# Optimization experiments

Hardware: AMD Instinct MI355X
Metric: run time of the kernel (lower is better)

## Reference

```python
import jax, jax.numpy as jnp
import numpy as np

HID = 16  # hidden channels of each lifting subnet (P and U)


def _conv(x, W, b):
    # x: [N,1|HID,h,w], W: [O,I,3,3] -> SAME conv, NCHW
    y = jax.lax.conv_general_dilated(x, W, (1, 1), 'SAME',
                                     dimension_numbers=('NCHW', 'OIHW', 'NCHW'))
    return y + b[None, :, None, None]


def _subnet(x, W1, b1, W2, b2):
    return _conv(jax.nn.relu(_conv(x, W1, b1)), W2, b2)


def _lift(L, H, p, u):
    # predict/update lifting step: H -= P(L); L += U(H)
    H = H - _subnet(L, *p)
    L = L + _subnet(H, *u)
    return L, H


def _rgb2yuv(x):
    # [B,3,H,W] -> YUV, then channels folded into batch -> [3B,1,H,W]
    M = jnp.array([[0.299, 0.587, 0.114],
                   [-0.147, -0.289, 0.436],
                   [0.615, -0.515, -0.100]], dtype=x.dtype)
    y = jnp.einsum('cd,bdhw->bchw', M, x)
    B, C, H, W = y.shape
    return y.transpose(1, 0, 2, 3).reshape(C * B, 1, H, W)


def _batch2channel(x, C):
    # [C*B,1,h,w] -> [B,C,h,w]  (inverse of the batch-fold above)
    CB, _, h, w = x.shape
    B = CB // C
    return x.reshape(C, B, h, w).transpose(1, 0, 2, 3)


def setup_inputs():
    key = jax.random.key(0)
    ks = jax.random.split(key, 5)
    B, H, W = 8, 512, 512
    x = jax.random.normal(ks[0], (B, 3, H, W), jnp.float32)

    def w(k, shape, fan):
        return jax.random.normal(k, shape, jnp.float32) * (1.0 / np.sqrt(fan))

    Wp1 = w(ks[1], (HID, 1, 3, 3), 9)
    bp1 = jnp.zeros((HID,), jnp.float32)
    Wp2 = w(ks[2], (1, HID, 3, 3), 9 * HID)
    bp2 = jnp.zeros((1,), jnp.float32)
    Wu1 = w(ks[3], (HID, 1, 3, 3), 9)
    bu1 = jnp.zeros((HID,), jnp.float32)
    Wu2 = w(ks[4], (1, HID, 3, 3), 9 * HID)
    bu2 = jnp.zeros((1,), jnp.float32)
    return dict(x=x, Wp1=Wp1, bp1=bp1, Wp2=Wp2, bp2=bp2,
                Wu1=Wu1, bu1=bu1, Wu2=Wu2, bu2=bu2)


def reference(x, Wp1, bp1, Wp2, bp2, Wu1, bu1, Wu2, bu2):
    p = (Wp1, bp1, Wp2, bp2)
    u = (Wu1, bu1, Wu2, bu2)
    C = x.shape[1]  # 3
    y = _rgb2yuv(x)                              # [3B,1,H,W]
    # level-1 vertical split + lifting
    L, Hb = y[:, :, 0::2, :], y[:, :, 1::2, :]   # [3B,1,H/2,W]
    L, Hb = _lift(L, Hb, p, u)
    # horizontal split of L
    Lt = L.transpose(0, 1, 3, 2)                 # [3B,1,W,H/2]
    LL, HL = Lt[:, :, 0::2, :], Lt[:, :, 1::2, :]
    LL, HL = _lift(LL, HL, p, u)
    LL = LL.transpose(0, 1, 3, 2)                # [3B,1,H/2,W/2]
    HL = HL.transpose(0, 1, 3, 2)
    # horizontal split of H
    Ht = Hb.transpose(0, 1, 3, 2)
    LH, HH = Ht[:, :, 0::2, :], Ht[:, :, 1::2, :]
    LH, HH = _lift(LH, HH, p, u)
    LH = LH.transpose(0, 1, 3, 2)
    HH = HH.transpose(0, 1, 3, 2)
    return jnp.concatenate([_batch2channel(t, C) for t in (LL, HL, LH, HH)],
                           axis=1)                # [B,12,H/2,W/2]
```

## Files before the change

kernel.cpp:

```cpp
#include <hip/hip_runtime.h>
#include <hip/hip_fp16.h>


#define P1 (24*256*512)

__device__ __forceinline__ __half2 oddpair(__half2 a, __half2 b) {
  unsigned ua = __builtin_bit_cast(unsigned, a), ub = __builtin_bit_cast(unsigned, b);
  unsigned r = __builtin_amdgcn_alignbit(ub, ua, 16);
  return __builtin_bit_cast(__half2, r);
}

__device__ __forceinline__ __half2 relu2(__half2 s) {
  unsigned u = __builtin_bit_cast(unsigned, s), r;
  asm("v_pk_max_f16 %0, %1, 0" : "=v"(r) : "v"(u));
  return __builtin_bit_cast(__half2, r);
}

template<int MODE>
__global__ __launch_bounds__(256, 4) void k_subnet(
    const float* __restrict__ xp, float* __restrict__ ws, float* __restrict__ outp,
    const float* __restrict__ W1, const float* __restrict__ B1,
    const float* __restrict__ W2, const float* __restrict__ B2)
{
  constexpr int  IW    = (MODE <= 1) ? 512 : 256;
  constexpr int  HW    = 256 * IW;
  constexpr float sign = (MODE == 0 || MODE == 2) ? -1.f : 1.f;
  constexpr int  TRANS = (MODE >= 2) ? 1 : 0;

  __shared__ __align__(16) __half2 sW[16*20];
  __shared__ __align__(16) __half  sIn[36*70];

  const int z     = blockIdx.z;
  const int n     = (MODE >= 2) ? (z % 24) : z;
  const int which = (MODE >= 2) ? (z / 24) : 0;
  const int c_ = n >> 3, b_ = n & 7;
  const int x0 = blockIdx.x * 64, y0 = blockIdx.y * 32;
  const int tid = threadIdx.x;
  float* Lw = ws;
  float* Hw = ws + P1;

  for (int i = tid; i < 320; i += 256) {
    int cc = i / 20, j = i - cc*20;
    float v = 0.f;
    if (j < 9)       { int jt = TRANS ? ((j%3)*3 + j/3) : j; v = W1[cc*9 + jt]; }
    else if (j == 9) v = B1[cc];
    else if (j < 19) { int k = j - 10; int jt = TRANS ? ((k%3)*3 + k/3) : k; v = W2[cc*9 + jt]; }
    __half h = __float2half(v);
    sW[i] = __halves2half2(h, h);
  }

  float m0 = 0.f, m1 = 0.f, m2 = 0.f;
  if (MODE == 0) {
    m0 = (c_==0) ? 0.299f : ((c_==1) ? -0.147f :  0.615f);
    m1 = (c_==0) ? 0.587f : ((c_==1) ? -0.289f : -0.515f);
    m2 = (c_==0) ? 0.114f : ((c_==1) ?  0.436f : -0.100f);
  }
  for (int i = tid; i < 36*68; i += 256) {
    int ly = i / 68, lx = i - ly*68;
    int gy = y0 + ly - 2, gx = x0 + lx - 2;
    float v = 0.f;
    if ((unsigned)gy < 256u && (unsigned)gx < (unsigned)IW) {
      if (MODE == 0) {
        const float* xb = xp + ((long)b_*3*512 + 2*gy)*512 + gx;
        v = m0*xb[0] + m1*xb[262144] + m2*xb[524288];
        Lw[(long)n*HW + gy*IW + gx] = v;
      } else if (MODE == 1) {
        v = Hw[(long)n*HW + gy*IW + gx];
      } else if (MODE == 2) {
        const float* s = (which ? Hw : Lw) + (long)n*(256*512);
        v = s[gy*512 + 2*gx];
      } else {
        const float* s = outp + (long)(b_*12 + (which?9:3) + c_)*65536;
        v = s[gy*256 + gx];
      }
    }
    sIn[ly*70 + lx] = __float2half(v);
  }
  __syncthreads();

  const int tx = tid & 15, ty = tid >> 4;
  const int oy = y0 + ty*2, ox = x0 + tx*4;

  __half2 E[6][4], O[6][3];
#pragma unroll
  for (int r = 0; r < 6; ++r) {
    const __half2* row = (const __half2*)&sIn[(ty*2 + r)*70 + tx*4];
    E[r][0] = row[0]; E[r][1] = row[1]; E[r][2] = row[2]; E[r][3] = row[3];
    O[r][0] = oddpair(E[r][0], E[r][1]);
    O[r][1] = oddpair(E[r][1], E[r][2]);
    O[r][2] = oddpair(E[r][2], E[r][3]);
  }

  const bool edgex = (x0 == 0) || (x0 + 64 == IW);
  bool rowok[4];
#pragma unroll
  for (int k = 0; k < 4; ++k) rowok[k] = ((unsigned)(oy - 1 + k) < 256u);
  __half2 mE[3];
  if (edgex) {
#pragma unroll
    for (int p = 0; p < 3; ++p) {
      float a = ((unsigned)(ox - 1 + 2*p) < (unsigned)IW) ? 1.f : 0.f;
      float b = ((unsigned)(ox     + 2*p) < (unsigned)IW) ? 1.f : 0.f;
      mE[p] = __halves2half2(__float2half(a), __float2half(b));
    }
  }

  const __half2 zero2 = __halves2half2(__float2half(0.f), __float2half(0.f));
  const __half2 negb  = __halves2half2(__float2half(-60000.f), __float2half(-60000.f));

  float   ACCF[2][4] = {{0,0,0,0},{0,0,0,0}};
  __half2 ACC2[2][2] = {{zero2, zero2},{zero2, zero2}};

#pragma unroll 1
  for (int c = 0; c < 16; ++c) {
    __half2 wv[20];
    const float4* wq = (const float4*)&sW[c*20];
#pragma unroll
    for (int q = 0; q < 5; ++q) {
      float4 f = wq[q];
      __half2 ph[4];
      ph[0] = __builtin_bit_cast(__half2, f.x);
      ph[1] = __builtin_bit_cast(__half2, f.y);
      ph[2] = __builtin_bit_cast(__half2, f.z);
      ph[3] = __builtin_bit_cast(__half2, f.w);
      wv[4*q+0] = ph[0]; wv[4*q+1] = ph[1]; wv[4*q+2] = ph[2]; wv[4*q+3] = ph[3];
    }
    __half2 bias[4];
#pragma unroll
    for (int k = 0; k < 4; ++k) bias[k] = rowok[k] ? wv[9] : negb;

#pragma unroll
    for (int k = 0; k < 4; ++k) {
      __half2 HE[3];
#pragma unroll
      for (int p = 0; p < 3; ++p) {
        __half2 s = bias[k];
#pragma unroll
        for (int dy = 0; dy < 3; ++dy) {
          s = __hfma2(wv[dy*3+0], E[k+dy][p],   s);
          s = __hfma2(wv[dy*3+1], O[k+dy][p],   s);
          s = __hfma2(wv[dy*3+2], E[k+dy][p+1], s);
        }
        HE[p] = relu2(s);
      }
      if (edgex) {
        HE[0] = __hmul2(HE[0], mE[0]);
        HE[1] = __hmul2(HE[1], mE[1]);
        HE[2] = __hmul2(HE[2], mE[2]);
      }
      __half2 HO0 = oddpair(HE[0], HE[1]);
      __half2 HO1 = oddpair(HE[1], HE[2]);
#pragma unroll
      for (int dy = 0; dy < 3; ++dy) {
        const int r = k - dy;
        if (r == 0 || r == 1) {
#pragma unroll
          for (int cp = 0; cp < 2; ++cp) {
            __half2 a = ACC2[r][cp];
            a = __hfma2(wv[10+dy*3+0], HE[cp],          a);
            a = __hfma2(wv[10+dy*3+1], (cp ? HO1 : HO0), a);
            a = __hfma2(wv[10+dy*3+2], HE[cp+1],        a);
            ACC2[r][cp] = a;
          }
        }
      }
    }
    if ((c & 3) == 3) {
#pragma unroll
      for (int r = 0; r < 2; ++r)
#pragma unroll
        for (int cp = 0; cp < 2; ++cp) {
          ACCF[r][2*cp]   += __low2float(ACC2[r][cp]);
          ACCF[r][2*cp+1] += __high2float(ACC2[r][cp]);
          ACC2[r][cp] = zero2;
        }
    }
  }

  const float b2 = B2[0];
  float4 iov[2];
  if (MODE == 0) {
#pragma unroll
    for (int r = 0; r < 2; ++r) {
      const float* xb = xp + ((long)b_*3*512 + (2*(oy+r)+1))*512 + ox;
      float4 rr = *(const float4*)&xb[0];
      float4 gg = *(const float4*)&xb[262144];
      float4 bb = *(const float4*)&xb[524288];
      iov[r] = make_float4(m0*rr.x + m1*gg.x + m2*bb.x,
                           m0*rr.y + m1*gg.y + m2*bb.y,
                           m0*rr.z + m1*gg.z + m2*bb.z,
                           m0*rr.w + m1*gg.w + m2*bb.w);
    }
  } else if (MODE == 1) {
    const float* s = Lw + (long)n*HW;
#pragma unroll
    for (int r = 0; r < 2; ++r) iov[r] = *(const float4*)&s[(oy+r)*IW + ox];
  } else {
    const float* s = (which ? Hw : Lw) + (long)n*(256*512);
#pragma unroll
    for (int r = 0; r < 2; ++r) {
      float4 a = *(const float4*)&s[(oy+r)*512 + 2*ox];
      float4 b = *(const float4*)&s[(oy+r)*512 + 2*ox + 4];
      iov[r] = (MODE == 2) ? make_float4(a.y, a.w, b.y, b.w)
                           : make_float4(a.x, a.z, b.x, b.z);
    }
  }

  float* dst;
  if      (MODE == 0) dst = Hw + (long)n*HW;
  else if (MODE == 1) dst = Lw + (long)n*HW;
  else if (MODE == 2) dst = outp + (long)(b_*12 + (which?9:3) + c_)*65536;
  else                dst = outp + (long)(b_*12 + (which?6:0) + c_)*65536;

#pragma unroll
  for (int r = 0; r < 2; ++r) {
    float4 v;
    v.x = iov[r].x + sign * (ACCF[r][0] + b2);
    v.y = iov[r].y + sign * (ACCF[r][1] + b2);
    v.z = iov[r].z + sign * (ACCF[r][2] + b2);
    v.w = iov[r].w + sign * (ACCF[r][3] + b2);
    *(float4*)&dst[(oy + r)*IW + ox] = v;
  }
}

extern "C" void kernel_launch(void* const* d_in, const int* in_sizes, int n_in,
                              void* d_out, int out_size, void* d_ws, size_t ws_size,
                              hipStream_t stream) {
  const float* x   = (const float*)d_in[0];
  const float* Wp1 = (const float*)d_in[1];
  const float* bp1 = (const float*)d_in[2];
  const float* Wp2 = (const float*)d_in[3];
  const float* bp2 = (const float*)d_in[4];
  const float* Wu1 = (const float*)d_in[5];
  const float* bu1 = (const float*)d_in[6];
  const float* Wu2 = (const float*)d_in[7];
  const float* bu2 = (const float*)d_in[8];
  float* out = (float*)d_out;
  float* ws  = (float*)d_ws;

  k_subnet<0><<<dim3(8,8,24), 256, 0, stream>>>(x, ws, out, Wp1, bp1, Wp2, bp2);
  k_subnet<1><<<dim3(8,8,24), 256, 0, stream>>>(x, ws, out, Wu1, bu1, Wu2, bu2);
  k_subnet<2><<<dim3(4,8,48), 256, 0, stream>>>(x, ws, out, Wp1, bp1, Wp2, bp2);
  k_subnet<3><<<dim3(4,8,48), 256, 0, stream>>>(x, ws, out, Wu1, bu1, Wu2, bu2);
}
```

Measured before the change: 260.6 us.

## Compute four output rows per thread to amortize hidden-layer halo recompute

```diff
diff --git a/kernel.cpp b/kernel.cpp
--- a/kernel.cpp
+++ b/kernel.cpp
@@ -17,7 +17,7 @@
 }
 
 template<int MODE>
-__global__ __launch_bounds__(256, 4) void k_subnet(
+__global__ __launch_bounds__(256, 3) void k_subnet(
     const float* __restrict__ xp, float* __restrict__ ws, float* __restrict__ outp,
     const float* __restrict__ W1, const float* __restrict__ B1,
     const float* __restrict__ W2, const float* __restrict__ B2)
@@ -28,13 +28,13 @@
   constexpr int  TRANS = (MODE >= 2) ? 1 : 0;
 
   __shared__ __align__(16) __half2 sW[16*20];
-  __shared__ __align__(16) __half  sIn[36*70];
+  __shared__ __align__(16) __half  sIn[68*72];
 
   const int z     = blockIdx.z;
   const int n     = (MODE >= 2) ? (z % 24) : z;
   const int which = (MODE >= 2) ? (z / 24) : 0;
   const int c_ = n >> 3, b_ = n & 7;
-  const int x0 = blockIdx.x * 64, y0 = blockIdx.y * 32;
+  const int x0 = blockIdx.x * 64, y0 = blockIdx.y * 64;
   const int tid = threadIdx.x;
   float* Lw = ws;
   float* Hw = ws + P1;
@@ -55,7 +55,7 @@
     m1 = (c_==0) ? 0.587f : ((c_==1) ? -0.289f : -0.515f);
     m2 = (c_==0) ? 0.114f : ((c_==1) ?  0.436f : -0.100f);
   }
-  for (int i = tid; i < 36*68; i += 256) {
+  for (int i = tid; i < 68*68; i += 256) {
     int ly = i / 68, lx = i - ly*68;
     int gy = y0 + ly - 2, gx = x0 + lx - 2;
     float v = 0.f;
@@ -74,17 +74,17 @@
         v = s[gy*256 + gx];
       }
     }
-    sIn[ly*70 + lx] = __float2half(v);
+    sIn[ly*72 + lx] = __float2half(v);
   }
   __syncthreads();
 
   const int tx = tid & 15, ty = tid >> 4;
-  const int oy = y0 + ty*2, ox = x0 + tx*4;
-
-  __half2 E[6][4], O[6][3];
-#pragma unroll
-  for (int r = 0; r < 6; ++r) {
-    const __half2* row = (const __half2*)&sIn[(ty*2 + r)*70 + tx*4];
+  const int oy = y0 + ty*4, ox = x0 + tx*4;
+
+  __half2 E[8][4], O[8][3];
+#pragma unroll
+  for (int r = 0; r < 8; ++r) {
+    const __half2* row = (const __half2*)&sIn[(ty*4 + r)*72 + tx*4];
     E[r][0] = row[0]; E[r][1] = row[1]; E[r][2] = row[2]; E[r][3] = row[3];
     O[r][0] = oddpair(E[r][0], E[r][1]);
     O[r][1] = oddpair(E[r][1], E[r][2]);
@@ -92,9 +92,9 @@
   }
 
   const bool edgex = (x0 == 0) || (x0 + 64 == IW);
-  bool rowok[4];
-#pragma unroll
-  for (int k = 0; k < 4; ++k) rowok[k] = ((unsigned)(oy - 1 + k) < 256u);
+  bool rowok[6];
+#pragma unroll
+  for (int k = 0; k < 6; ++k) rowok[k] = ((unsigned)(oy - 1 + k) < 256u);
   __half2 mE[3];
   if (edgex) {
 #pragma unroll
@@ -105,11 +105,11 @@
     }
   }
 
-  const __half2 zero2 = __halves2half2(__float2half(0.f), __float2half(0.f));
+  const __half2 zero2 = __builtin_bit_cast(__half2, 0u);
   const __half2 negb  = __halves2half2(__float2half(-60000.f), __float2half(-60000.f));
 
-  float   ACCF[2][4] = {{0,0,0,0},{0,0,0,0}};
-  __half2 ACC2[2][2] = {{zero2, zero2},{zero2, zero2}};
+  float   ACCF[4][4] = {{0,0,0,0},{0,0,0,0},{0,0,0,0},{0,0,0,0}};
+  __half2 ACC2[4][2] = {{zero2,zero2},{zero2,zero2},{zero2,zero2},{zero2,zero2}};
 
 #pragma unroll 1
   for (int c = 0; c < 16; ++c) {
@@ -118,30 +118,28 @@
 #pragma unroll
     for (int q = 0; q < 5; ++q) {
       float4 f = wq[q];
-      __half2 ph[4];
-      ph[0] = __builtin_bit_cast(__half2, f.x);
-      ph[1] = __builtin_bit_cast(__half2, f.y);
-      ph[2] = __builtin_bit_cast(__half2, f.z);
-      ph[3] = __builtin_bit_cast(__half2, f.w);
-      wv[4*q+0] = ph[0]; wv[4*q+1] = ph[1]; wv[4*q+2] = ph[2]; wv[4*q+3] = ph[3];
-    }
-    __half2 bias[4];
-#pragma unroll
-    for (int k = 0; k < 4; ++k) bias[k] = rowok[k] ? wv[9] : negb;
-
-#pragma unroll
-    for (int k = 0; k < 4; ++k) {
+      wv[4*q+0] = __builtin_bit_cast(__half2, f.x);
+      wv[4*q+1] = __builtin_bit_cast(__half2, f.y);
+      wv[4*q+2] = __builtin_bit_cast(__half2, f.z);
+      wv[4*q+3] = __builtin_bit_cast(__half2, f.w);
+    }
+    __half2 bias[6];
+#pragma unroll
+    for (int k = 0; k < 6; ++k) bias[k] = rowok[k] ? wv[9] : negb;
+
+#pragma unroll
+    for (int kk = 0; kk < 6; ++kk) {
       __half2 HE[3];
 #pragma unroll
       for (int p = 0; p < 3; ++p) {
-        __half2 s = bias[k];
+        __half2 hs = bias[kk];
 #pragma unroll
         for (int dy = 0; dy < 3; ++dy) {
-          s = __hfma2(wv[dy*3+0], E[k+dy][p],   s);
-          s = __hfma2(wv[dy*3+1], O[k+dy][p],   s);
-          s = __hfma2(wv[dy*3+2], E[k+dy][p+1], s);
+          hs = __hfma2(wv[dy*3+0], E[kk+dy][p],   hs);
+          hs = __hfma2(wv[dy*3+1], O[kk+dy][p],   hs);
+          hs = __hfma2(wv[dy*3+2], E[kk+dy][p+1], hs);
         }
-        HE[p] = relu2(s);
+        HE[p] = relu2(hs);
       }
       if (edgex) {
         HE[0] = __hmul2(HE[0], mE[0]);
@@ -152,14 +150,14 @@
       __half2 HO1 = oddpair(HE[1], HE[2]);
 #pragma unroll
       for (int dy = 0; dy < 3; ++dy) {
-        const int r = k - dy;
-        if (r == 0 || r == 1) {
+        const int r = kk - dy;
+        if (r >= 0 && r < 4) {
 #pragma unroll
           for (int cp = 0; cp < 2; ++cp) {
             __half2 a = ACC2[r][cp];
-            a = __hfma2(wv[10+dy*3+0], HE[cp],          a);
+            a = __hfma2(wv[10+dy*3+0], HE[cp],           a);
             a = __hfma2(wv[10+dy*3+1], (cp ? HO1 : HO0), a);
-            a = __hfma2(wv[10+dy*3+2], HE[cp+1],        a);
+            a = __hfma2(wv[10+dy*3+2], HE[cp+1],         a);
             ACC2[r][cp] = a;
           }
         }
@@ -167,7 +165,7 @@
     }
     if ((c & 3) == 3) {
 #pragma unroll
-      for (int r = 0; r < 2; ++r)
+      for (int r = 0; r < 4; ++r)
 #pragma unroll
         for (int cp = 0; cp < 2; ++cp) {
           ACCF[r][2*cp]   += __low2float(ACC2[r][cp]);
@@ -178,10 +176,10 @@
   }
 
   const float b2 = B2[0];
-  float4 iov[2];
+  float4 iov[4];
   if (MODE == 0) {
 #pragma unroll
-    for (int r = 0; r < 2; ++r) {
+    for (int r = 0; r < 4; ++r) {
       const float* xb = xp + ((long)b_*3*512 + (2*(oy+r)+1))*512 + ox;
       float4 rr = *(const float4*)&xb[0];
       float4 gg = *(const float4*)&xb[262144];
@@ -194,11 +192,11 @@
   } else if (MODE == 1) {
     const float* s = Lw + (long)n*HW;
 #pragma unroll
-    for (int r = 0; r < 2; ++r) iov[r] = *(const float4*)&s[(oy+r)*IW + ox];
+    for (int r = 0; r < 4; ++r) iov[r] = *(const float4*)&s[(oy+r)*IW + ox];
   } else {
     const float* s = (which ? Hw : Lw) + (long)n*(256*512);
 #pragma unroll
-    for (int r = 0; r < 2; ++r) {
+    for (int r = 0; r < 4; ++r) {
       float4 a = *(const float4*)&s[(oy+r)*512 + 2*ox];
       float4 b = *(const float4*)&s[(oy+r)*512 + 2*ox + 4];
       iov[r] = (MODE == 2) ? make_float4(a.y, a.w, b.y, b.w)
@@ -213,7 +211,7 @@
   else                dst = outp + (long)(b_*12 + (which?6:0) + c_)*65536;
 
 #pragma unroll
-  for (int r = 0; r < 2; ++r) {
+  for (int r = 0; r < 4; ++r) {
     float4 v;
     v.x = iov[r].x + sign * (ACCF[r][0] + b2);
     v.y = iov[r].y + sign * (ACCF[r][1] + b2);
@@ -238,8 +236,8 @@
   float* out = (float*)d_out;
   float* ws  = (float*)d_ws;
 
-  k_subnet<0><<<dim3(8,8,24), 256, 0, stream>>>(x, ws, out, Wp1, bp1, Wp2, bp2);
-  k_subnet<1><<<dim3(8,8,24), 256, 0, stream>>>(x, ws, out, Wu1, bu1, Wu2, bu2);
-  k_subnet<2><<<dim3(4,8,48), 256, 0, stream>>>(x, ws, out, Wp1, bp1, Wp2, bp2);
-  k_subnet<3><<<dim3(4,8,48), 256, 0, stream>>>(x, ws, out, Wu1, bu1, Wu2, bu2);
-}
+  k_subnet<0><<<dim3(8,4,24), 256, 0, stream>>>(x, ws, out, Wp1, bp1, Wp2, bp2);
+  k_subnet<1><<<dim3(8,4,24), 256, 0, stream>>>(x, ws, out, Wu1, bu1, Wu2, bu2);
+  k_subnet<2><<<dim3(4,4,48), 256, 0, stream>>>(x, ws, out, Wp1, bp1, Wp2, bp2);
+  k_subnet<3><<<dim3(4,4,48), 256, 0, stream>>>(x, ws, out, Wu1, bu1, Wu2, bu2);
+}
```

Result: faster. 245.2 us (-5.9%).
